# Kernel optimization log

Measured on AMD Instinct MI355X. Metric: run time of the kernel, lower is better.

Reference implementation:

```python
import jax, jax.numpy as jnp
import numpy as np

N_NODES = 100000
N_EDGES = 1600000
D_IN = 256
D_HID = 128
N_CLASSES = 64
NEG_SLOPE = 0.2


def setup_inputs() -> dict:
    key = jax.random.key(0)
    ks = jax.random.split(key, 8)
    node_features = jax.random.normal(ks[0], (N_NODES, D_IN), dtype=jnp.float32)
    W = jax.random.normal(ks[1], (D_IN, D_HID), dtype=jnp.float32) * (1.0 / np.sqrt(D_IN))
    attn_l = jax.random.normal(ks[2], (D_HID,), dtype=jnp.float32) * (1.0 / np.sqrt(D_HID))
    attn_r = jax.random.normal(ks[3], (D_HID,), dtype=jnp.float32) * (1.0 / np.sqrt(D_HID))
    fc_W = jax.random.normal(ks[4], (D_HID, N_CLASSES), dtype=jnp.float32) * (1.0 / np.sqrt(D_HID))
    fc_b = jnp.zeros((N_CLASSES,), dtype=jnp.float32)
    src = jax.random.randint(ks[5], (N_EDGES,), 0, N_NODES, dtype=jnp.int32)
    dst = jax.random.randint(ks[6], (N_EDGES,), 0, N_NODES, dtype=jnp.int32)
    return dict(node_features=node_features, W=W, attn_l=attn_l, attn_r=attn_r,
                fc_W=fc_W, fc_b=fc_b, src=src, dst=dst)


def reference(node_features, W, attn_l, attn_r, fc_W, fc_b, src, dst):
    N = node_features.shape[0]
    # GATConv (single head): linear projection
    feat = node_features @ W                       # [N, H]
    el = feat @ attn_l                             # [N]
    er = feat @ attn_r                             # [N]
    e = jax.nn.leaky_relu(el[src] + er[dst], NEG_SLOPE)  # [E]
    # segment softmax over incoming edges of each destination node
    m = jax.ops.segment_max(e, dst, num_segments=N)      # [N]
    ex = jnp.exp(e - m[dst])                              # [E]
    denom = jax.ops.segment_sum(ex, dst, num_segments=N)  # [N]
    a = ex / denom[dst]                                   # [E]
    # attention-weighted neighbor aggregation (scatter-add)
    msg = a[:, None] * feat[src]                           # [E, H]
    h = jax.ops.segment_sum(msg, dst, num_segments=N)     # [N, H]
    # num_heads=1 -> h.mean(1) over heads is identity; final Linear
    return h @ fc_W + fc_b                                 # [N, C]
```

## Files before the change

### kernel.cpp

```cpp
#include <hip/hip_runtime.h>
#include <math.h>

#define NN 100000
#define NE 1600000
#define DIN 256
#define DHID 128
#define NCLS 64
#define NEG_SLOPE 0.2f

#define NBUCK 196
#define ECAP 10240
#define CHUNK 4096
#define NCHB ((NE + CHUNK - 1) / CHUNK)
#define PREPB 32

#define NGRP 32768
#define G1 ((NN + 127) / 128)

typedef __bf16 bf16_t;
typedef bf16_t bf16x8 __attribute__((ext_vector_type(8)));
typedef float f32x4 __attribute__((ext_vector_type(4)));
typedef ushort ushort8v __attribute__((ext_vector_type(8)));
typedef ushort ushort4v __attribute__((ext_vector_type(4)));

__device__ __forceinline__ ushort f2bf(float f) {
    union { float f; unsigned u; } c; c.f = f;
    unsigned u = c.u;
    unsigned r = (u + 0x7FFFu + ((u >> 16) & 1u)) >> 16;
    return (ushort)r;
}
__device__ __forceinline__ float bf2f(ushort b) {
    return __uint_as_float(((unsigned)b) << 16);
}

union SmemA {
    struct {
        int hist[NBUCK];
        int scn[256];
        int loff[NBUCK];
        int cur[NBUCK];
        int gb[NBUCK];
        unsigned ord[CHUNK];
        ushort obk[CHUNK];
    } b;
};

__global__ __launch_bounds__(256) void fused_a(const int* __restrict__ src,
                                               const int* __restrict__ dst,
                                               int* __restrict__ gcur,
                                               unsigned* __restrict__ ebuf,
                                               const float* __restrict__ W,
                                               const float* __restrict__ fcW,
                                               ushort* __restrict__ Wt,
                                               ushort* __restrict__ fcWt) {
    __shared__ SmemA sm;
    const int t = threadIdx.x;

    if (blockIdx.x >= NCHB) {
        int t0 = (blockIdx.x - NCHB) * 256 + t;
        for (int i = t0; i < DHID * DIN; i += PREPB * 256) {
            int n = i >> 8, k = i & 255;
            Wt[i] = f2bf(W[k * DHID + n]);
        }
        for (int i = t0; i < NCLS * DHID; i += PREPB * 256) {
            int n = i >> 7, k = i & 127;
            fcWt[i] = f2bf(fcW[k * NCLS + n]);
        }
        return;
    }

    const int base = blockIdx.x * CHUNK;
    int cnt = NE - base; if (cnt > CHUNK) cnt = CHUNK;

    for (int i = t; i < NBUCK; i += 256) sm.b.hist[i] = 0;
    __syncthreads();

    unsigned vals[16];
    int bks[16];
#pragma unroll
    for (int i = 0; i < 16; i++) {
        int idx = base + i * 256 + t;
        if (idx < NE) {
            int d = dst[idx], s = src[idx];
            int bb = d >> 9;
            bks[i] = bb;
            vals[i] = ((unsigned)(d & 511) << 17) | (unsigned)s;
            atomicAdd(&sm.b.hist[bb], 1);
        } else bks[i] = -1;
    }
    __syncthreads();

    int hv = (t < NBUCK) ? sm.b.hist[t] : 0;
    sm.b.scn[t] = hv;
    __syncthreads();
    for (int d = 1; d < 256; d <<= 1) {
        int a = (t >= d) ? sm.b.scn[t - d] : 0;
        __syncthreads();
        sm.b.scn[t] += a;
        __syncthreads();
    }
    if (t < NBUCK) { sm.b.loff[t] = sm.b.scn[t] - hv; sm.b.cur[t] = sm.b.scn[t] - hv; }
    __syncthreads();

#pragma unroll
    for (int i = 0; i < 16; i++) {
        if (bks[i] >= 0) {
            int slot = atomicAdd(&sm.b.cur[bks[i]], 1);
            sm.b.ord[slot] = vals[i];
            sm.b.obk[slot] = (ushort)bks[i];
        }
    }
    if (t < NBUCK && hv > 0) sm.b.gb[t] = t * ECAP + atomicAdd(&gcur[t], hv);
    __syncthreads();

    for (int s = t; s < cnt; s += 256) {
        int bb = sm.b.obk[s];
        ebuf[sm.b.gb[bb] + (s - sm.b.loff[bb])] = sm.b.ord[s];
    }
}

union SmemB {
    struct {
        ushort Xs[2][8192];
        ushort Wl[2][8192];
        float Al[DHID];
        float Ar[DHID];
    } g;
    struct {
        int sdeg[512];
        int pr[256];
        int lofs[512];
        int scnt[512];
    } c;
    int sh[256];
};

__global__ __launch_bounds__(256, 2) void fused_b(const float* __restrict__ X,
                                                  const ushort* __restrict__ Wt,
                                                  const float* __restrict__ attn_l,
                                                  const float* __restrict__ attn_r,
                                                  ushort* __restrict__ featb,
                                                  float* __restrict__ el,
                                                  float* __restrict__ er,
                                                  const unsigned* __restrict__ ebuf,
                                                  const int* __restrict__ gcur,
                                                  int* __restrict__ off_g,
                                                  int* __restrict__ deg_g,
                                                  int* __restrict__ ssrc,
                                                  int* __restrict__ bpre) {
    __shared__ SmemB sm;
    const int t = threadIdx.x;

    if (blockIdx.x >= G1 + NBUCK) {
        int v = (t < NBUCK) ? gcur[t] : 0;
        sm.sh[t] = v;
        __syncthreads();
        for (int d = 1; d < 256; d <<= 1) {
            int a = (t >= d) ? sm.sh[t - d] : 0;
            __syncthreads();
            sm.sh[t] += a;
            __syncthreads();
        }
        if (t < NBUCK) bpre[t] = sm.sh[t] - v;
        if (t == NBUCK - 1) bpre[NBUCK] = sm.sh[t];
        return;
    }

    if (blockIdx.x >= G1) {
        const int b = blockIdx.x - G1;
        const int node0 = b << 9;
        const int ebase = b * ECAP;
        const int ecnt = gcur[b];

        sm.c.sdeg[t] = 0; sm.c.sdeg[t + 256] = 0;
        __syncthreads();
        for (int s = t; s < ecnt; s += 256)
            atomicAdd(&sm.c.sdeg[ebuf[ebase + s] >> 17], 1);
        __syncthreads();

        int d0 = sm.c.sdeg[2 * t], d1 = sm.c.sdeg[2 * t + 1];
        sm.c.pr[t] = d0 + d1;
        __syncthreads();
        for (int d = 1; d < 256; d <<= 1) {
            int a = (t >= d) ? sm.c.pr[t - d] : 0;
            __syncthreads();
            sm.c.pr[t] += a;
            __syncthreads();
        }
        int ex = sm.c.pr[t] - d0 - d1;
        sm.c.lofs[2 * t] = ex;
        sm.c.lofs[2 * t + 1] = ex + d0;
        sm.c.scnt[2 * t] = 0; sm.c.scnt[2 * t + 1] = 0;
        int n0 = node0 + 2 * t, n1 = n0 + 1;
        if (n0 < NN) { off_g[n0] = ebase + ex;      deg_g[n0] = d0; }
        if (n1 < NN) { off_g[n1] = ebase + ex + d0; deg_g[n1] = d1; }
        __syncthreads();

        for (int s = t; s < ecnt; s += 256) {
            unsigned v = ebuf[ebase + s];
            int dl = v >> 17;
            int c = atomicAdd(&sm.c.scnt[dl], 1);
            ssrc[ebase + sm.c.lofs[dl] + c] = (int)(v & 0x1FFFFu);
        }
        return;
    }

    const int row0 = blockIdx.x * 128;
    if (t < 128) { sm.g.Al[t] = attn_l[t]; sm.g.Ar[t] = attn_r[t]; }

    int srow[4], ske[4];
#pragma unroll
    for (int i = 0; i < 4; i++) {
        int o = i * 4096 + t * 16;
        int row = o >> 7;
        int bl = (o & 127) ^ ((row & 7) << 4);
        srow[i] = row;
        ske[i] = bl >> 1;
    }

    float4 xr[4][2];
    uint4  wr[4];

#pragma unroll
    for (int i = 0; i < 4; i++) {
        int grow = row0 + srow[i];
        if (grow < NN) {
            const float4* p = (const float4*)(X + (size_t)grow * DIN + ske[i]);
            xr[i][0] = p[0]; xr[i][1] = p[1];
        } else {
            xr[i][0] = make_float4(0.f, 0.f, 0.f, 0.f);
            xr[i][1] = make_float4(0.f, 0.f, 0.f, 0.f);
        }
        wr[i] = *(const uint4*)(Wt + (size_t)srow[i] * DIN + ske[i]);
    }
#pragma unroll
    for (int i = 0; i < 4; i++) {
        int o = i * 4096 + t * 16;
        ushort8v b;
        b[0] = f2bf(xr[i][0].x); b[1] = f2bf(xr[i][0].y);
        b[2] = f2bf(xr[i][0].z); b[3] = f2bf(xr[i][0].w);
        b[4] = f2bf(xr[i][1].x); b[5] = f2bf(xr[i][1].y);
        b[6] = f2bf(xr[i][1].z); b[7] = f2bf(xr[i][1].w);
        *(ushort8v*)((char*)&sm.g.Xs[0][0] + o) = b;
        *(uint4*)((char*)&sm.g.Wl[0][0] + o) = wr[i];
    }
    __syncthreads();

    const int w = t >> 6, lane = t & 63;
    const int rbase = w * 32;
    const int lcol = lane & 15;
    const int kgrp = (lane >> 4) * 16;

    f32x4 acc[2][8];
#pragma unroll
    for (int r = 0; r < 2; r++)
#pragma unroll
        for (int c = 0; c < 8; c++) acc[r][c] = (f32x4){0.f, 0.f, 0.f, 0.f};

    for (int c = 0; c < 4; c++) {
        const int buf = c & 1;
        if (c < 3) {
            int k0g = (c + 1) * 64;
#pragma unroll
            for (int i = 0; i < 4; i++) {
                int grow = row0 + srow[i];
                if (grow < NN) {
                    const float4* p = (const float4*)(X + (size_t)grow * DIN + k0g + ske[i]);
                    xr[i][0] = p[0]; xr[i][1] = p[1];
                } else {
                    xr[i][0] = make_float4(0.f, 0.f, 0.f, 0.f);
                    xr[i][1] = make_float4(0.f, 0.f, 0.f, 0.f);
                }
                wr[i] = *(const uint4*)(Wt + (size_t)srow[i] * DIN + k0g + ske[i]);
            }
        }
        const char* xb = (const char*)&sm.g.Xs[buf][0];
        const char* wb = (const char*)&sm.g.Wl[buf][0];
#pragma unroll
        for (int k0 = 0; k0 < 2; k0++) {
            int kb = k0 * 64 + kgrp;
            bf16x8 a[2], b[8];
#pragma unroll
            for (int r = 0; r < 2; r++) {
                int row = rbase + r * 16 + lcol;
                a[r] = *(const bf16x8*)(xb + row * 128 + (kb ^ ((row & 7) << 4)));
            }
#pragma unroll
            for (int cc = 0; cc < 8; cc++) {
                int n = cc * 16 + lcol;
                b[cc] = *(const bf16x8*)(wb + n * 128 + (kb ^ ((n & 7) << 4)));
            }
#pragma unroll
            for (int r = 0; r < 2; r++)
#pragma unroll
                for (int cc = 0; cc < 8; cc++)
                    acc[r][cc] = __builtin_amdgcn_mfma_f32_16x16x32_bf16(a[r], b[cc], acc[r][cc], 0, 0, 0);
        }
        if (c < 3) {
#pragma unroll
            for (int i = 0; i < 4; i++) {
                int o = i * 4096 + t * 16;
                ushort8v b;
                b[0] = f2bf(xr[i][0].x); b[1] = f2bf(xr[i][0].y);
                b[2] = f2bf(xr[i][0].z); b[3] = f2bf(xr[i][0].w);
                b[4] = f2bf(xr[i][1].x); b[5] = f2bf(xr[i][1].y);
                b[6] = f2bf(xr[i][1].z); b[7] = f2bf(xr[i][1].w);
                *(ushort8v*)((char*)&sm.g.Xs[buf ^ 1][0] + o) = b;
                *(uint4*)((char*)&sm.g.Wl[buf ^ 1][0] + o) = wr[i];
            }
        }
        __syncthreads();
    }

    ushort* Os = (ushort*)sm.g.Xs;
#pragma unroll
    for (int r = 0; r < 2; r++)
#pragma unroll
        for (int cc = 0; cc < 8; cc++)
#pragma unroll
            for (int i = 0; i < 4; i++) {
                int rloc = rbase + r * 16 + (lane >> 4) * 4 + i;
                int col = cc * 16 + lcol;
                Os[rloc * 128 + col] = f2bf(acc[r][cc][i]);
            }
    __syncthreads();

    {
        int row = t >> 1, half = t & 1;
        int grow = row0 + row;
        const ushort* orow = Os + row * 128 + half * 64;
        const float* alp = sm.g.Al + half * 64;
        const float* arp = sm.g.Ar + half * 64;
        float pl = 0.f, pr = 0.f;
        int rot = row & 7;
#pragma unroll
        for (int qq = 0; qq < 8; qq++) {
            int q = (qq + rot) & 7;
            ushort8v f8 = *(const ushort8v*)(orow + q * 8);
#pragma unroll
            for (int e = 0; e < 8; e++) {
                float fe = bf2f(f8[e]);
                pl += fe * alp[q * 8 + e];
                pr += fe * arp[q * 8 + e];
            }
        }
        pl += __shfl_down(pl, 1);
        pr += __shfl_down(pr, 1);
        if (!half && grow < NN) { el[grow] = pl; er[grow] = pr; }
    }

#pragma unroll
    for (int i = 0; i < 8; i++) {
        int u = i * 256 + t;
        int row = u >> 4;
        int grow = row0 + row;
        if (grow < NN)
            *(uint4*)(featb + (size_t)grow * 128 + (u & 15) * 8) =
                *(uint4*)((char*)Os + u * 16);
    }
}

__global__ __launch_bounds__(256) void k_split(const int* __restrict__ off,
                                               const int* __restrict__ bpre,
                                               int* __restrict__ nsplit) {
    int g = blockIdx.x * 256 + threadIdx.x;
    if (g > NGRP) return;
    if (g == NGRP) { nsplit[NGRP] = NN; return; }
    long total = bpre[NBUCK];
    long target = (long)g * total / NGRP;
    int lo = 0, hi = NN;
    while (lo < hi) {
        int mid = (lo + hi) >> 1;
        int b = mid >> 9;
        long real = (long)off[mid] - (long)b * ECAP + bpre[b];
        if (real < target) lo = mid + 1; else hi = mid;
    }
    nsplit[g] = lo;
}

__global__ __launch_bounds__(256) void aggregate(const int* __restrict__ off,
                                                 const int* __restrict__ deg,
                                                 const int* __restrict__ ssrc,
                                                 const float* __restrict__ el,
                                                 const float* __restrict__ er,
                                                 const ushort* __restrict__ featb,
                                                 ushort* __restrict__ hb,
                                                 const int* __restrict__ nsplit) {
    const int half = blockIdx.x & 1;
    const int gid = (blockIdx.x >> 1) * 16 + (threadIdx.x >> 4);
    const int lc = threadIdx.x & 15;
    int n = nsplit[gid];
    const int nend = nsplit[gid + 1];
    const ushort* fb = featb + half * 64 + lc * 4;
    ushort* hbh = hb + half * 64 + lc * 4;

    for (; n < nend; ++n) {
        const int e0 = off[n];
        const int dg = deg[n];
        const float erd = er[n];
        float acc0 = 0.f, acc1 = 0.f, acc2 = 0.f, acc3 = 0.f;
        float wsum = 0.f;

        int j = 0;
        for (; j + 8 <= dg; j += 8) {
            int sv[8];
            ushort4v fv[8];
            float wv[8];
#pragma unroll
            for (int u = 0; u < 8; u++) sv[u] = ssrc[e0 + j + u];
#pragma unroll
            for (int u = 0; u < 8; u++)
                fv[u] = *(const ushort4v*)(fb + (size_t)sv[u] * DHID);
#pragma unroll
            for (int u = 0; u < 8; u++) {
                float x = el[sv[u]] + erd;
                x = x > 0.f ? x : NEG_SLOPE * x;
                wv[u] = __expf(x);
                wsum += wv[u];
            }
#pragma unroll
            for (int u = 0; u < 8; u++) {
                acc0 += wv[u] * bf2f(fv[u][0]);
                acc1 += wv[u] * bf2f(fv[u][1]);
                acc2 += wv[u] * bf2f(fv[u][2]);
                acc3 += wv[u] * bf2f(fv[u][3]);
            }
        }
        for (; j < dg; ++j) {
            int s0 = ssrc[e0 + j];
            ushort4v f0 = *(const ushort4v*)(fb + (size_t)s0 * DHID);
            float x0 = el[s0] + erd;
            x0 = x0 > 0.f ? x0 : NEG_SLOPE * x0;
            float w0 = __expf(x0);
            wsum += w0;
            acc0 += w0 * bf2f(f0[0]);
            acc1 += w0 * bf2f(f0[1]);
            acc2 += w0 * bf2f(f0[2]);
            acc3 += w0 * bf2f(f0[3]);
        }

        float inv = (dg > 0) ? 1.0f / wsum : 0.f;
        ushort4v o4;
        o4[0] = f2bf(acc0 * inv);
        o4[1] = f2bf(acc1 * inv);
        o4[2] = f2bf(acc2 * inv);
        o4[3] = f2bf(acc3 * inv);
        *(ushort4v*)(hbh + (size_t)n * DHID) = o4;
    }
}

__global__ __launch_bounds__(256) void gemm2(const ushort* __restrict__ hb,
                                             const ushort* __restrict__ fcWt,
                                             const float* __restrict__ fcb,
                                             float* __restrict__ out) {
    __shared__ ushort Hs[128 * 128];
    __shared__ ushort Fs[64 * 128];
    const int t = threadIdx.x;
    const int row0 = blockIdx.x * 128;

    {
#pragma unroll
        for (int i = 0; i < 8; i++) {
            int u = i * 256 + t;
            int row = u >> 4;
            int grow = row0 + row;
            uint4 v = make_uint4(0, 0, 0, 0);
            if (grow < NN) v = *(const uint4*)(hb + (size_t)grow * 128 + (u & 15) * 8);
            int byte_off = row * 256 + (((u & 15) * 16) ^ ((row & 7) << 4));
            *(uint4*)((char*)Hs + byte_off) = v;
        }
#pragma unroll
        for (int i = 0; i < 4; i++) {
            int u = i * 256 + t;
            int n = u >> 4;
            int byte_off = n * 256 + (((u & 15) * 16) ^ ((n & 7) << 4));
            *(uint4*)((char*)Fs + byte_off) = ((const uint4*)fcWt)[u];
        }
    }

    const int w = t >> 6, lane = t & 63;
    const int rbase = w * 32;
    const int lcol = lane & 15;
    const int kgrp = (lane >> 4) * 16;

    f32x4 acc[2][4];
#pragma unroll
    for (int c = 0; c < 4; c++) {
        float bias = fcb[c * 16 + lcol];
#pragma unroll
        for (int r = 0; r < 2; r++)
#pragma unroll
            for (int i = 0; i < 4; i++) acc[r][c][i] = bias;
    }
    __syncthreads();

#pragma unroll
    for (int k0 = 0; k0 < 4; k0++) {
        int kbyte = k0 * 64 + kgrp;
        bf16x8 a[2], b[4];
#pragma unroll
        for (int r = 0; r < 2; r++) {
            int row = rbase + r * 16 + lcol;
            a[r] = *(bf16x8*)((char*)Hs + row * 256 + (kbyte ^ ((row & 7) << 4)));
        }
#pragma unroll
        for (int c = 0; c < 4; c++) {
            int n = c * 16 + lcol;
            b[c] = *(bf16x8*)((char*)Fs + n * 256 + (kbyte ^ ((n & 7) << 4)));
        }
#pragma unroll
        for (int r = 0; r < 2; r++)
#pragma unroll
            for (int c = 0; c < 4; c++)
                acc[r][c] = __builtin_amdgcn_mfma_f32_16x16x32_bf16(a[r], b[c], acc[r][c], 0, 0, 0);
    }

#pragma unroll
    for (int r = 0; r < 2; r++)
#pragma unroll
        for (int i = 0; i < 4; i++) {
            int row = rbase + r * 16 + (lane >> 4) * 4 + i;
            int grow = row0 + row;
            if (grow < NN) {
                float* op = out + (size_t)grow * 64 + lcol;
#pragma unroll
                for (int c = 0; c < 4; c++) op[c * 16] = acc[r][c][i];
            }
        }
}

extern "C" void kernel_launch(void* const* d_in, const int* in_sizes, int n_in,
                              void* d_out, int out_size, void* d_ws, size_t ws_size,
                              hipStream_t stream) {
    const float* X      = (const float*)d_in[0];
    const float* W      = (const float*)d_in[1];
    const float* attn_l = (const float*)d_in[2];
    const float* attn_r = (const float*)d_in[3];
    const float* fcW    = (const float*)d_in[4];
    const float* fcb    = (const float*)d_in[5];
    const int*   src    = (const int*)d_in[6];
    const int*   dst    = (const int*)d_in[7];
    float* out = (float*)d_out;

    char* ws = (char*)d_ws;
    ushort* featb = (ushort*)ws;            ws += (size_t)NN * DHID * 2;
    ushort* hb    = (ushort*)ws;            ws += (size_t)NN * DHID * 2;
    ushort* Wt    = (ushort*)ws;            ws += (size_t)DHID * DIN * 2;
    ushort* fcWt  = (ushort*)ws;            ws += (size_t)NCLS * DHID * 2;
    float* el     = (float*)ws;             ws += (size_t)NN * 4;
    float* er     = (float*)ws;             ws += (size_t)NN * 4;
    int*   deg    = (int*)ws;               ws += (size_t)NN * 4;
    int*   off    = (int*)ws;               ws += (size_t)NN * 4;
    int*   ssrc   = (int*)ws;               ws += (size_t)NBUCK * ECAP * 4;
    unsigned* ebuf = (unsigned*)ws;         ws += (size_t)NBUCK * ECAP * 4;
    int*   gcur   = (int*)ws;               ws += (size_t)256 * 4;
    int*   bpre   = (int*)ws;               ws += (size_t)256 * 4;
    int*   nsplit = (int*)ws;               ws += (size_t)(NGRP + 1) * 4;

    hipMemsetAsync(gcur, 0, NBUCK * sizeof(int), stream);

    fused_a<<<NCHB + PREPB, 256, 0, stream>>>(src, dst, gcur, ebuf, W, fcW, Wt, fcWt);
    fused_b<<<G1 + NBUCK + 1, 256, 0, stream>>>(X, Wt, attn_l, attn_r, featb, el, er,
                                                ebuf, gcur, off, deg, ssrc, bpre);
    k_split<<<(NGRP + 256) / 256, 256, 0, stream>>>(off, bpre, nsplit);
    aggregate<<<(NGRP / 16) * 2, 256, 0, stream>>>(off, deg, ssrc, el, er, featb, hb, nsplit);
    gemm2<<<(NN + 127) / 128, 256, 0, stream>>>(hb, fcWt, fcb, out);
}
```

Before: 170.6 us.

## Restructure pipeline: fuse binning with GEMM1, inline split search, widen aggregate lanes

Weight prep and zeroing of the bucket counters now run in a small prep kernel, which removes the memset. Edge binning is merged into the GEMM1 kernel, and CSR building moves to its own kernel. The separate split kernel is removed and each aggregate group does its own binary search for its node range. Aggregate now has each 16-lane group cover all 128 features with 8-wide loads instead of splitting into two halves, using half as many groups and a 4-edge unroll. The intent is fewer launches and gathering each source row once instead of twice, at the cost of a redundant binary search per group and more registers.

After: 160.4 us. 1.06x faster.

```diff
diff --git a/kernel.cpp b/kernel.cpp
--- a/kernel.cpp
+++ b/kernel.cpp
@@ -12,16 +12,15 @@
 #define ECAP 10240
 #define CHUNK 4096
 #define NCHB ((NE + CHUNK - 1) / CHUNK)
-#define PREPB 32
-
-#define NGRP 32768
+#define PREPB 16
+
+#define NGRP 16384
 #define G1 ((NN + 127) / 128)
 
 typedef __bf16 bf16_t;
 typedef bf16_t bf16x8 __attribute__((ext_vector_type(8)));
 typedef float f32x4 __attribute__((ext_vector_type(4)));
 typedef ushort ushort8v __attribute__((ext_vector_type(8)));
-typedef ushort ushort4v __attribute__((ext_vector_type(4)));
 
 __device__ __forceinline__ ushort f2bf(float f) {
     union { float f; unsigned u; } c; c.f = f;
@@ -33,7 +32,24 @@
     return __uint_as_float(((unsigned)b) << 16);
 }
 
-union SmemA {
+__global__ __launch_bounds__(256) void k_prep(const float* __restrict__ W,
+                                              const float* __restrict__ fcW,
+                                              ushort* __restrict__ Wt,
+                                              ushort* __restrict__ fcWt,
+                                              int* __restrict__ gcur) {
+    int t = blockIdx.x * 256 + threadIdx.x;
+    if (blockIdx.x == 0) gcur[threadIdx.x] = 0;
+    for (int i = t; i < DHID * DIN; i += PREPB * 256) {
+        int n = i >> 8, k = i & 255;
+        Wt[i] = f2bf(W[k * DHID + n]);
+    }
+    for (int i = t; i < NCLS * DHID; i += PREPB * 256) {
+        int n = i >> 7, k = i & 127;
+        fcWt[i] = f2bf(fcW[k * NCLS + n]);
+    }
+}
+
+union SmemB {
     struct {
         int hist[NBUCK];
         int scn[256];
@@ -43,169 +59,76 @@
         unsigned ord[CHUNK];
         ushort obk[CHUNK];
     } b;
-};
-
-__global__ __launch_bounds__(256) void fused_a(const int* __restrict__ src,
-                                               const int* __restrict__ dst,
-                                               int* __restrict__ gcur,
-                                               unsigned* __restrict__ ebuf,
-                                               const float* __restrict__ W,
-                                               const float* __restrict__ fcW,
-                                               ushort* __restrict__ Wt,
-                                               ushort* __restrict__ fcWt) {
-    __shared__ SmemA sm;
-    const int t = threadIdx.x;
-
-    if (blockIdx.x >= NCHB) {
-        int t0 = (blockIdx.x - NCHB) * 256 + t;
-        for (int i = t0; i < DHID * DIN; i += PREPB * 256) {
-            int n = i >> 8, k = i & 255;
-            Wt[i] = f2bf(W[k * DHID + n]);
-        }
-        for (int i = t0; i < NCLS * DHID; i += PREPB * 256) {
-            int n = i >> 7, k = i & 127;
-            fcWt[i] = f2bf(fcW[k * NCLS + n]);
-        }
-        return;
-    }
-
-    const int base = blockIdx.x * CHUNK;
-    int cnt = NE - base; if (cnt > CHUNK) cnt = CHUNK;
-
-    for (int i = t; i < NBUCK; i += 256) sm.b.hist[i] = 0;
-    __syncthreads();
-
-    unsigned vals[16];
-    int bks[16];
-#pragma unroll
-    for (int i = 0; i < 16; i++) {
-        int idx = base + i * 256 + t;
-        if (idx < NE) {
-            int d = dst[idx], s = src[idx];
-            int bb = d >> 9;
-            bks[i] = bb;
-            vals[i] = ((unsigned)(d & 511) << 17) | (unsigned)s;
-            atomicAdd(&sm.b.hist[bb], 1);
-        } else bks[i] = -1;
-    }
-    __syncthreads();
-
-    int hv = (t < NBUCK) ? sm.b.hist[t] : 0;
-    sm.b.scn[t] = hv;
-    __syncthreads();
-    for (int d = 1; d < 256; d <<= 1) {
-        int a = (t >= d) ? sm.b.scn[t - d] : 0;
-        __syncthreads();
-        sm.b.scn[t] += a;
-        __syncthreads();
-    }
-    if (t < NBUCK) { sm.b.loff[t] = sm.b.scn[t] - hv; sm.b.cur[t] = sm.b.scn[t] - hv; }
-    __syncthreads();
-
-#pragma unroll
-    for (int i = 0; i < 16; i++) {
-        if (bks[i] >= 0) {
-            int slot = atomicAdd(&sm.b.cur[bks[i]], 1);
-            sm.b.ord[slot] = vals[i];
-            sm.b.obk[slot] = (ushort)bks[i];
-        }
-    }
-    if (t < NBUCK && hv > 0) sm.b.gb[t] = t * ECAP + atomicAdd(&gcur[t], hv);
-    __syncthreads();
-
-    for (int s = t; s < cnt; s += 256) {
-        int bb = sm.b.obk[s];
-        ebuf[sm.b.gb[bb] + (s - sm.b.loff[bb])] = sm.b.ord[s];
-    }
-}
-
-union SmemB {
     struct {
         ushort Xs[2][8192];
         ushort Wl[2][8192];
         float Al[DHID];
         float Ar[DHID];
     } g;
-    struct {
-        int sdeg[512];
-        int pr[256];
-        int lofs[512];
-        int scnt[512];
-    } c;
-    int sh[256];
 };
 
-__global__ __launch_bounds__(256, 2) void fused_b(const float* __restrict__ X,
-                                                  const ushort* __restrict__ Wt,
-                                                  const float* __restrict__ attn_l,
-                                                  const float* __restrict__ attn_r,
-                                                  ushort* __restrict__ featb,
-                                                  float* __restrict__ el,
-                                                  float* __restrict__ er,
-                                                  const unsigned* __restrict__ ebuf,
-                                                  const int* __restrict__ gcur,
-                                                  int* __restrict__ off_g,
-                                                  int* __restrict__ deg_g,
-                                                  int* __restrict__ ssrc,
-                                                  int* __restrict__ bpre) {
+__global__ __launch_bounds__(256, 2) void fused_bin_gemm1(
+        const int* __restrict__ src, const int* __restrict__ dst,
+        int* __restrict__ gcur, unsigned* __restrict__ ebuf,
+        const float* __restrict__ X, const ushort* __restrict__ Wt,
+        const float* __restrict__ attn_l, const float* __restrict__ attn_r,
+        ushort* __restrict__ featb, float* __restrict__ el, float* __restrict__ er) {
     __shared__ SmemB sm;
     const int t = threadIdx.x;
 
-    if (blockIdx.x >= G1 + NBUCK) {
-        int v = (t < NBUCK) ? gcur[t] : 0;
-        sm.sh[t] = v;
+    if (blockIdx.x < NCHB) {
+        const int base = blockIdx.x * CHUNK;
+        int cnt = NE - base; if (cnt > CHUNK) cnt = CHUNK;
+
+        for (int i = t; i < NBUCK; i += 256) sm.b.hist[i] = 0;
+        __syncthreads();
+
+        unsigned vals[16];
+        int bks[16];
+#pragma unroll
+        for (int i = 0; i < 16; i++) {
+            int idx = base + i * 256 + t;
+            if (idx < NE) {
+                int d = dst[idx], s = src[idx];
+                int bb = d >> 9;
+                bks[i] = bb;
+                vals[i] = ((unsigned)(d & 511) << 17) | (unsigned)s;
+                atomicAdd(&sm.b.hist[bb], 1);
+            } else bks[i] = -1;
+        }
+        __syncthreads();
+
+        int hv = (t < NBUCK) ? sm.b.hist[t] : 0;
+        sm.b.scn[t] = hv;
         __syncthreads();
         for (int d = 1; d < 256; d <<= 1) {
-            int a = (t >= d) ? sm.sh[t - d] : 0;
+            int a = (t >= d) ? sm.b.scn[t - d] : 0;
             __syncthreads();
-            sm.sh[t] += a;
+            sm.b.scn[t] += a;
             __syncthreads();
         }
-        if (t < NBUCK) bpre[t] = sm.sh[t] - v;
-        if (t == NBUCK - 1) bpre[NBUCK] = sm.sh[t];
+        if (t < NBUCK) { sm.b.loff[t] = sm.b.scn[t] - hv; sm.b.cur[t] = sm.b.scn[t] - hv; }
+        __syncthreads();
+
+#pragma unroll
+        for (int i = 0; i < 16; i++) {
+            if (bks[i] >= 0) {
+                int slot = atomicAdd(&sm.b.cur[bks[i]], 1);
+                sm.b.ord[slot] = vals[i];
+                sm.b.obk[slot] = (ushort)bks[i];
+            }
+        }
+        if (t < NBUCK && hv > 0) sm.b.gb[t] = t * ECAP + atomicAdd(&gcur[t], hv);
+        __syncthreads();
+
+        for (int s = t; s < cnt; s += 256) {
+            int bb = sm.b.obk[s];
+            ebuf[sm.b.gb[bb] + (s - sm.b.loff[bb])] = sm.b.ord[s];
+        }
         return;
     }
 
-    if (blockIdx.x >= G1) {
-        const int b = blockIdx.x - G1;
-        const int node0 = b << 9;
-        const int ebase = b * ECAP;
-        const int ecnt = gcur[b];
-
-        sm.c.sdeg[t] = 0; sm.c.sdeg[t + 256] = 0;
-        __syncthreads();
-        for (int s = t; s < ecnt; s += 256)
-            atomicAdd(&sm.c.sdeg[ebuf[ebase + s] >> 17], 1);
-        __syncthreads();
-
-        int d0 = sm.c.sdeg[2 * t], d1 = sm.c.sdeg[2 * t + 1];
-        sm.c.pr[t] = d0 + d1;
-        __syncthreads();
-        for (int d = 1; d < 256; d <<= 1) {
-            int a = (t >= d) ? sm.c.pr[t - d] : 0;
-            __syncthreads();
-            sm.c.pr[t] += a;
-            __syncthreads();
-        }
-        int ex = sm.c.pr[t] - d0 - d1;
-        sm.c.lofs[2 * t] = ex;
-        sm.c.lofs[2 * t + 1] = ex + d0;
-        sm.c.scnt[2 * t] = 0; sm.c.scnt[2 * t + 1] = 0;
-        int n0 = node0 + 2 * t, n1 = n0 + 1;
-        if (n0 < NN) { off_g[n0] = ebase + ex;      deg_g[n0] = d0; }
-        if (n1 < NN) { off_g[n1] = ebase + ex + d0; deg_g[n1] = d1; }
-        __syncthreads();
-
-        for (int s = t; s < ecnt; s += 256) {
-            unsigned v = ebuf[ebase + s];
-            int dl = v >> 17;
-            int c = atomicAdd(&sm.c.scnt[dl], 1);
-            ssrc[ebase + sm.c.lofs[dl] + c] = (int)(v & 0x1FFFFu);
-        }
-        return;
-    }
-
-    const int row0 = blockIdx.x * 128;
+    const int row0 = (blockIdx.x - NCHB) * 128;
     if (t < 128) { sm.g.Al[t] = attn_l[t]; sm.g.Ar[t] = attn_r[t]; }
 
     int srow[4], ske[4];
@@ -360,14 +283,80 @@
     }
 }
 
-__global__ __launch_bounds__(256) void k_split(const int* __restrict__ off,
-                                               const int* __restrict__ bpre,
-                                               int* __restrict__ nsplit) {
-    int g = blockIdx.x * 256 + threadIdx.x;
-    if (g > NGRP) return;
-    if (g == NGRP) { nsplit[NGRP] = NN; return; }
-    long total = bpre[NBUCK];
-    long target = (long)g * total / NGRP;
+union SmemC {
+    struct {
+        int sdeg[512];
+        int pr[256];
+        int lofs[512];
+        int scnt[512];
+    } c;
+    int sh[256];
+};
+
+__global__ __launch_bounds__(256) void fused_csr(const unsigned* __restrict__ ebuf,
+                                                 const int* __restrict__ gcur,
+                                                 int* __restrict__ off_g,
+                                                 int* __restrict__ deg_g,
+                                                 int* __restrict__ ssrc,
+                                                 int* __restrict__ bpre) {
+    __shared__ SmemC sm;
+    const int t = threadIdx.x;
+
+    if (blockIdx.x == NBUCK) {
+        int v = (t < NBUCK) ? gcur[t] : 0;
+        sm.sh[t] = v;
+        __syncthreads();
+        for (int d = 1; d < 256; d <<= 1) {
+            int a = (t >= d) ? sm.sh[t - d] : 0;
+            __syncthreads();
+            sm.sh[t] += a;
+            __syncthreads();
+        }
+        if (t < NBUCK) bpre[t] = sm.sh[t] - v;
+        if (t == NBUCK - 1) bpre[NBUCK] = sm.sh[t];
+        return;
+    }
+
+    const int b = blockIdx.x;
+    const int node0 = b << 9;
+    const int ebase = b * ECAP;
+    const int ecnt = gcur[b];
+
+    sm.c.sdeg[t] = 0; sm.c.sdeg[t + 256] = 0;
+    __syncthreads();
+    for (int s = t; s < ecnt; s += 256)
+        atomicAdd(&sm.c.sdeg[ebuf[ebase + s] >> 17], 1);
+    __syncthreads();
+
+    int d0 = sm.c.sdeg[2 * t], d1 = sm.c.sdeg[2 * t + 1];
+    sm.c.pr[t] = d0 + d1;
+    __syncthreads();
+    for (int d = 1; d < 256; d <<= 1) {
+        int a = (t >= d) ? sm.c.pr[t - d] : 0;
+        __syncthreads();
+        sm.c.pr[t] += a;
+        __syncthreads();
+    }
+    int ex = sm.c.pr[t] - d0 - d1;
+    sm.c.lofs[2 * t] = ex;
+    sm.c.lofs[2 * t + 1] = ex + d0;
+    sm.c.scnt[2 * t] = 0; sm.c.scnt[2 * t + 1] = 0;
+    int n0 = node0 + 2 * t, n1 = n0 + 1;
+    if (n0 < NN) { off_g[n0] = ebase + ex;      deg_g[n0] = d0; }
+    if (n1 < NN) { off_g[n1] = ebase + ex + d0; deg_g[n1] = d1; }
+    __syncthreads();
+
+    for (int s = t; s < ecnt; s += 256) {
+        unsigned v = ebuf[ebase + s];
+        int dl = v >> 17;
+        int c = atomicAdd(&sm.c.scnt[dl], 1);
+        ssrc[ebase + sm.c.lofs[dl] + c] = (int)(v & 0x1FFFFu);
+    }
+}
+
+__device__ __forceinline__ int find_node(const int* __restrict__ off,
+                                         const int* __restrict__ bpre,
+                                         long target) {
     int lo = 0, hi = NN;
     while (lo < hi) {
         int mid = (lo + hi) >> 1;
@@ -375,7 +364,7 @@
         long real = (long)off[mid] - (long)b * ECAP + bpre[b];
         if (real < target) lo = mid + 1; else hi = mid;
     }
-    nsplit[g] = lo;
+    return lo;
 }
 
 __global__ __launch_bounds__(256) void aggregate(const int* __restrict__ off,
@@ -385,67 +374,63 @@
                                                  const float* __restrict__ er,
                                                  const ushort* __restrict__ featb,
                                                  ushort* __restrict__ hb,
-                                                 const int* __restrict__ nsplit) {
-    const int half = blockIdx.x & 1;
-    const int gid = (blockIdx.x >> 1) * 16 + (threadIdx.x >> 4);
+                                                 const int* __restrict__ bpre) {
+    const int gid = blockIdx.x * 16 + (threadIdx.x >> 4);
     const int lc = threadIdx.x & 15;
-    int n = nsplit[gid];
-    const int nend = nsplit[gid + 1];
-    const ushort* fb = featb + half * 64 + lc * 4;
-    ushort* hbh = hb + half * 64 + lc * 4;
+    const long total = bpre[NBUCK];
+    int n = find_node(off, bpre, (long)gid * total / NGRP);
+    const int nend = find_node(off, bpre, (long)(gid + 1) * total / NGRP);
+    const ushort* fb = featb + lc * 8;
 
     for (; n < nend; ++n) {
         const int e0 = off[n];
         const int dg = deg[n];
         const float erd = er[n];
-        float acc0 = 0.f, acc1 = 0.f, acc2 = 0.f, acc3 = 0.f;
+        float acc[8];
+#pragma unroll
+        for (int q = 0; q < 8; q++) acc[q] = 0.f;
         float wsum = 0.f;
 
         int j = 0;
-        for (; j + 8 <= dg; j += 8) {
-            int sv[8];
-            ushort4v fv[8];
-            float wv[8];
-#pragma unroll
-            for (int u = 0; u < 8; u++) sv[u] = ssrc[e0 + j + u];
-#pragma unroll
-            for (int u = 0; u < 8; u++)
-                fv[u] = *(const ushort4v*)(fb + (size_t)sv[u] * DHID);
-#pragma unroll
-            for (int u = 0; u < 8; u++) {
-                float x = el[sv[u]] + erd;
-                x = x > 0.f ? x : NEG_SLOPE * x;
-                wv[u] = __expf(x);
-                wsum += wv[u];
-            }
-#pragma unroll
-            for (int u = 0; u < 8; u++) {
-                acc0 += wv[u] * bf2f(fv[u][0]);
-                acc1 += wv[u] * bf2f(fv[u][1]);
-                acc2 += wv[u] * bf2f(fv[u][2]);
-                acc3 += wv[u] * bf2f(fv[u][3]);
-            }
+        for (; j + 4 <= dg; j += 4) {
+            int s0 = ssrc[e0 + j + 0];
+            int s1 = ssrc[e0 + j + 1];
+            int s2 = ssrc[e0 + j + 2];
+            int s3 = ssrc[e0 + j + 3];
+            ushort8v f0 = *(const ushort8v*)(fb + (size_t)s0 * DHID);
+            ushort8v f1 = *(const ushort8v*)(fb + (size_t)s1 * DHID);
+            ushort8v f2 = *(const ushort8v*)(fb + (size_t)s2 * DHID);
+            ushort8v f3 = *(const ushort8v*)(fb + (size_t)s3 * DHID);
+            float x0 = el[s0] + erd, x1 = el[s1] + erd;
+            float x2 = el[s2] + erd, x3 = el[s3] + erd;
+            x0 = x0 > 0.f ? x0 : NEG_SLOPE * x0;
+            x1 = x1 > 0.f ? x1 : NEG_SLOPE * x1;
+            x2 = x2 > 0.f ? x2 : NEG_SLOPE * x2;
+            x3 = x3 > 0.f ? x3 : NEG_SLOPE * x3;
+            float w0 = __expf(x0), w1 = __expf(x1);
+            float w2 = __expf(x2), w3 = __expf(x3);
+            wsum += (w0 + w1) + (w2 + w3);
+#pragma unroll
+            for (int q = 0; q < 8; q++)
+                acc[q] += (w0 * bf2f(f0[q]) + w1 * bf2f(f1[q])) +
+                          (w2 * bf2f(f2[q]) + w3 * bf2f(f3[q]));
         }
         for (; j < dg; ++j) {
             int s0 = ssrc[e0 + j];
-            ushort4v f0 = *(const ushort4v*)(fb + (size_t)s0 * DHID);
+            ushort8v f0 = *(const ushort8v*)(fb + (size_t)s0 * DHID);
             float x0 = el[s0] + erd;
             x0 = x0 > 0.f ? x0 : NEG_SLOPE * x0;
             float w0 = __expf(x0);
             wsum += w0;
-            acc0 += w0 * bf2f(f0[0]);
-            acc1 += w0 * bf2f(f0[1]);
-            acc2 += w0 * bf2f(f0[2]);
-            acc3 += w0 * bf2f(f0[3]);
+#pragma unroll
+            for (int q = 0; q < 8; q++) acc[q] += w0 * bf2f(f0[q]);
         }
 
         float inv = (dg > 0) ? 1.0f / wsum : 0.f;
-        ushort4v o4;
-        o4[0] = f2bf(acc0 * inv);
-        o4[1] = f2bf(acc1 * inv);
-        o4[2] = f2bf(acc2 * inv);
-        o4[3] = f2bf(acc3 * inv);
-        *(ushort4v*)(hbh + (size_t)n * DHID) = o4;
+        ushort8v o8;
+#pragma unroll
+        for (int q = 0; q < 8; q++) o8[q] = f2bf(acc[q] * inv);
+        *(ushort8v*)(hb + (size_t)n * DHID + lc * 8) = o8;
     }
 }
 
@@ -555,14 +540,11 @@
     unsigned* ebuf = (unsigned*)ws;         ws += (size_t)NBUCK * ECAP * 4;
     int*   gcur   = (int*)ws;               ws += (size_t)256 * 4;
     int*   bpre   = (int*)ws;               ws += (size_t)256 * 4;
-    int*   nsplit = (int*)ws;               ws += (size_t)(NGRP + 1) * 4;
-
-    hipMemsetAsync(gcur, 0, NBUCK * sizeof(int), stream);
-
-    fused_a<<<NCHB + PREPB, 256, 0, stream>>>(src, dst, gcur, ebuf, W, fcW, Wt, fcWt);
-    fused_b<<<G1 + NBUCK + 1, 256, 0, stream>>>(X, Wt, attn_l, attn_r, featb, el, er,
-                                                ebuf, gcur, off, deg, ssrc, bpre);
-    k_split<<<(NGRP + 256) / 256, 256, 0, stream>>>(off, bpre, nsplit);
-    aggregate<<<(NGRP / 16) * 2, 256, 0, stream>>>(off, deg, ssrc, el, er, featb, hb, nsplit);
+
+    k_prep<<<PREPB, 256, 0, stream>>>(W, fcW, Wt, fcWt, gcur);
+    fused_bin_gemm1<<<NCHB + G1, 256, 0, stream>>>(src, dst, gcur, ebuf,
+                                                   X, Wt, attn_l, attn_r, featb, el, er);
+    fused_csr<<<NBUCK + 1, 256, 0, stream>>>(ebuf, gcur, off, deg, ssrc, bpre);
+    aggregate<<<NGRP / 16, 256, 0, stream>>>(off, deg, ssrc, el, er, featb, hb, bpre);
     gemm2<<<(NN + 127) / 128, 256, 0, stream>>>(hb, fcWt, fcb, out);
 }
```
